# Performance work log

Measured on AMD Instinct MI355X. Metric: run time of the kernel, lower is better.

The kernel has to match this reference:

```python
import jax, jax.numpy as jnp
import numpy as np

L, B, D = 2048, 2, 1024
H, DK, DV = 16, 64, 64
SPAN = 128
LN_EPS = 1e-5


def setup_inputs() -> dict:
    key = jax.random.key(0)
    ks = jax.random.split(key, 8)
    s_qk = np.sqrt(2.0 / (D + DK)).astype(np.float32)
    s_v = np.sqrt(2.0 / (D + DV)).astype(np.float32)
    return {
        "query": jax.random.normal(ks[0], (L, B, D), jnp.float32),
        "key": jax.random.normal(ks[1], (L, B, D), jnp.float32),
        "value": jax.random.normal(ks[2], (L, B, D), jnp.float32),
        "Wq": jax.random.normal(ks[3], (D, H * DK), jnp.float32) * s_qk,
        "bq": jnp.zeros((H * DK,), jnp.float32),
        "Wk": jax.random.normal(ks[4], (D, H * DK), jnp.float32) * s_qk,
        "bk": jnp.zeros((H * DK,), jnp.float32),
        "Wv": jax.random.normal(ks[5], (D, H * DV), jnp.float32) * s_v,
        "bv": jnp.zeros((H * DV,), jnp.float32),
        "Wfc": jax.random.normal(ks[6], (H * DV, D), jnp.float32) * np.sqrt(2.0 / (H * DV + D)).astype(np.float32),
        "bfc": jnp.zeros((D,), jnp.float32),
        "gamma": jnp.ones((D,), jnp.float32),
        "beta": jnp.zeros((D,), jnp.float32),
    }


def reference(query, key, value, Wq, bq, Wk, bk, Wv, bv, Wfc, bfc, gamma, beta):
    l, b, d = query.shape
    # projections: (l,b,H*dk) -> (H,b,l,dk)   [torch rearrange 'l b (head k) -> head b l k']
    q = (query @ Wq + bq).reshape(l, b, H, DK).transpose(2, 1, 0, 3)
    k = (key @ Wk + bk).reshape(l, b, H, DK).transpose(2, 1, 0, 3)
    v = (value @ Wv + bv).reshape(l, b, H, DV).transpose(2, 1, 0, 3)
    scores = jnp.einsum("hblk,hbtk->hblt", q, k) / jnp.sqrt(jnp.float32(DK))
    # banded additive mask: keep |j - i| <= SPAN
    idx = jnp.arange(l)
    band = jnp.abs(idx[None, :] - idx[:, None]) <= SPAN  # (l, l)
    scores = jnp.where(band[None, None], scores, -jnp.inf)
    attn = jax.nn.softmax(scores, axis=-1)
    out = jnp.einsum("hblt,hbtv->hblv", attn, v)
    # 'head b l v -> l b (head v)'
    out = out.transpose(2, 1, 0, 3).reshape(l, b, H * DV)
    out = out @ Wfc + bfc  # dropout p=0.0 -> identity
    y = out + query  # residual
    mu = jnp.mean(y, axis=-1, keepdims=True)
    var = jnp.mean(jnp.square(y - mu), axis=-1, keepdims=True)
    y = (y - mu) * jax.lax.rsqrt(var + LN_EPS) * gamma + beta
    return (y, attn)
```

## Files before the change

kernel.cpp:

```cpp
#include <hip/hip_runtime.h>
#include <stdint.h>

#define L_SEQ 2048
#define BB 2
#define DD 1024
#define NH 16
#define SPAN 128

typedef __attribute__((ext_vector_type(8))) short short8;
typedef __attribute__((ext_vector_type(4))) float floatx4;

__device__ __forceinline__ short f32_bf16(float f) {
  uint32_t u = __float_as_uint(f);
  u += 0x7FFFu + ((u >> 16) & 1u);
  return (short)(u >> 16);
}
__device__ __forceinline__ float bf2f(short s) {
  return __uint_as_float(((uint32_t)(uint16_t)s) << 16);
}

__device__ __forceinline__ void gld16(const short* g, short* l) {
  __builtin_amdgcn_global_load_lds(
      (__attribute__((address_space(1))) void*)(g),
      (__attribute__((address_space(3))) void*)(l), 16, 0, 0);
}

__global__ __launch_bounds__(256) void k_prep(
    const float* __restrict__ s0, const float* __restrict__ s1, const float* __restrict__ s2,
    const float* __restrict__ w0, const float* __restrict__ w1,
    const float* __restrict__ w2, const float* __restrict__ w3,
    short* __restrict__ d0, short* __restrict__ d1, short* __restrict__ d2,
    short* __restrict__ WT) {
  __shared__ float tile[32][33];
  int bid = blockIdx.x, tid = threadIdx.x;
  if (bid < 12288) {
    int y = bid >> 12;
    const float* s = y == 0 ? s0 : (y == 1 ? s1 : s2);
    short* d = y == 0 ? d0 : (y == 1 ? d1 : d2);
    int i = (bid & 4095) * 256 + tid;
    float4 v = ((const float4*)s)[i];
    short4 o;
    o.x = f32_bf16(v.x); o.y = f32_bf16(v.y); o.z = f32_bf16(v.z); o.w = f32_bf16(v.w);
    ((short4*)d)[i] = o;
  } else {
    int b2 = bid - 12288;
    int z = b2 >> 10;
    int xy = b2 & 1023;
    int bx = (xy & 31) * 32, by = (xy >> 5) * 32;
    int tx = tid & 31, ty = tid >> 5;
    const float* src = z == 0 ? w0 : z == 1 ? w1 : z == 2 ? w2 : w3;
    short* out = WT + (size_t)z * (DD * DD);
#pragma unroll
    for (int r = 0; r < 32; r += 8)
      tile[ty + r][tx] = src[(size_t)(by + ty + r) * DD + bx + tx];
    __syncthreads();
#pragma unroll
    for (int r = 0; r < 32; r += 8)
      out[(size_t)(bx + ty + r) * DD + by + tx] = f32_bf16(tile[tx][ty + r]);
  }
}

#define BM 128
#define BN 128

__device__ __forceinline__ void gemm_core(const short* __restrict__ A,
                                          const short* __restrict__ BT,
                                          floatx4 acc[4][4], int bm0, int bn0) {
  __shared__ short As0[BM * 32], As1[BM * 32];
  __shared__ short Bs0[BN * 32], Bs1[BN * 32];
  int tid = threadIdx.x;
  int wave = tid >> 6, lane = tid & 63;
  int li = lane & 15, quad = lane >> 4;
  int wm = (wave & 1) * 64, wn = (wave >> 1) * 64;
  int r0 = wave * 32 + (lane >> 2);
  int c0 = (lane & 3) * 8;
  const short* gA = A + (size_t)(bm0 + r0) * DD + c0;
  const short* gB = BT + (size_t)(bn0 + r0) * DD + c0;
  short* lA0 = &As0[wave * 32 * 32];
  short* lA1 = &As1[wave * 32 * 32];
  short* lB0 = &Bs0[wave * 32 * 32];
  short* lB1 = &Bs1[wave * 32 * 32];
  for (int k0 = 0; k0 < DD; k0 += 64) {
    __syncthreads();
    gld16(gA + k0, lA0);
    gld16(gA + (size_t)16 * DD + k0, lA0 + 16 * 32);
    gld16(gA + k0 + 32, lA1);
    gld16(gA + (size_t)16 * DD + k0 + 32, lA1 + 16 * 32);
    gld16(gB + k0, lB0);
    gld16(gB + (size_t)16 * DD + k0, lB0 + 16 * 32);
    gld16(gB + k0 + 32, lB1);
    gld16(gB + (size_t)16 * DD + k0 + 32, lB1 + 16 * 32);
    __syncthreads();
    short8 af[4], bf[4];
#pragma unroll
    for (int t = 0; t < 4; ++t) {
      af[t] = *(const short8*)&As0[(wm + t * 16 + li) * 32 + quad * 8];
      bf[t] = *(const short8*)&Bs0[(wn + t * 16 + li) * 32 + quad * 8];
    }
#pragma unroll
    for (int tm = 0; tm < 4; ++tm)
#pragma unroll
      for (int tn = 0; tn < 4; ++tn)
        acc[tm][tn] = __builtin_amdgcn_mfma_f32_16x16x32_bf16(af[tm], bf[tn], acc[tm][tn], 0, 0, 0);
#pragma unroll
    for (int t = 0; t < 4; ++t) {
      af[t] = *(const short8*)&As1[(wm + t * 16 + li) * 32 + quad * 8];
      bf[t] = *(const short8*)&Bs1[(wn + t * 16 + li) * 32 + quad * 8];
    }
#pragma unroll
    for (int tm = 0; tm < 4; ++tm)
#pragma unroll
      for (int tn = 0; tn < 4; ++tn)
        acc[tm][tn] = __builtin_amdgcn_mfma_f32_16x16x32_bf16(af[tm], bf[tn], acc[tm][tn], 0, 0, 0);
  }
}

__global__ __launch_bounds__(256) void k_proj(
    const short* __restrict__ xq, const short* __restrict__ xk, const short* __restrict__ xv,
    const short* __restrict__ WT,
    const float* __restrict__ bq, const float* __restrict__ bk, const float* __restrict__ bv,
    short* __restrict__ qo, short* __restrict__ ko, short* __restrict__ vo) {
  int mode = blockIdx.z;
  const short* A = mode == 0 ? xq : (mode == 1 ? xk : xv);
  const short* BT = WT + (size_t)mode * DD * DD;
  const float* bias = mode == 0 ? bq : (mode == 1 ? bk : bv);
  floatx4 acc[4][4] = {};
  int bm0 = blockIdx.y * BM, bn0 = blockIdx.x * BN;
  gemm_core(A, BT, acc, bm0, bn0);

  int tid = threadIdx.x;
  int wave = tid >> 6, lane = tid & 63;
  int li = lane & 15, quad = lane >> 4;
  int wm = (wave & 1) * 64, wn = (wave >> 1) * 64;
  short* dst = (mode == 0) ? qo : (mode == 1 ? ko : vo);
#pragma unroll
  for (int tm = 0; tm < 4; ++tm) {
#pragma unroll
    for (int tn = 0; tn < 4; ++tn) {
      int gn = bn0 + wn + tn * 16 + li;
      float bs = bias[gn];
      int h = gn >> 6, dk = gn & 63;
#pragma unroll
      for (int r = 0; r < 4; ++r) {
        int gm = bm0 + wm + tm * 16 + quad * 4 + r;
        int l = gm >> 1, b = gm & 1;
        dst[(((size_t)h * BB + b) * L_SEQ + l) * 64 + dk] = f32_bf16(acc[tm][tn][r] + bs);
      }
    }
  }
}

__global__ __launch_bounds__(256) void k_vt(const short* __restrict__ vl, short* __restrict__ vt) {
  __shared__ short tl[64][72];
  int l0 = blockIdx.x * 64, hb = blockIdx.y;
  const short* src = vl + ((size_t)hb * L_SEQ + l0) * 64;
  short* dst = vt + (size_t)hb * 64 * L_SEQ + l0;
  int tid = threadIdx.x;
  int r = tid >> 2, c0 = (tid & 3) * 16;
  *(short8*)&tl[r][c0] = *(const short8*)(src + (size_t)r * 64 + c0);
  *(short8*)&tl[r][c0 + 8] = *(const short8*)(src + (size_t)r * 64 + c0 + 8);
  __syncthreads();
  int d = tid >> 2, lb = (tid & 3) * 16;
  short8 o0, o1;
#pragma unroll
  for (int j = 0; j < 8; ++j) o0[j] = tl[lb + j][d];
#pragma unroll
  for (int j = 0; j < 8; ++j) o1[j] = tl[lb + 8 + j][d];
  *(short8*)(dst + (size_t)d * L_SEQ + lb) = o0;
  *(short8*)(dst + (size_t)d * L_SEQ + lb + 8) = o1;
}

__global__ __launch_bounds__(256) void k_attn(
    const short* __restrict__ qw, const short* __restrict__ kw, const short* __restrict__ vTw,
    float* __restrict__ attn_out, short* __restrict__ ctx) {
  __shared__ short sbuf[20480];
  short* K0 = sbuf;
  short* K1 = sbuf + 10240;
  const int tid = threadIdx.x;
  const int wv = tid >> 6, lane = tid & 63;
  const int li = lane & 15, quad = lane >> 4;
  const int i0b = blockIdx.x * 64;
  const int i0 = i0b + wv * 16;
  const int jb = i0b - SPAN;
  const int hb = blockIdx.y;
  const short* Q = qw + (size_t)hb * L_SEQ * 64;
  const short* K = kw + (size_t)hb * L_SEQ * 64;
  const short* VT = vTw + (size_t)hb * 64 * L_SEQ;
  float* Aout = attn_out + (size_t)hb * L_SEQ * L_SEQ;

#pragma unroll
  for (int t = 0; t < 10; ++t) {
    int idx = wv + 4 * t;
    int half = idx >= 20 ? 1 : 0;
    int ridx = idx - half * 20;
    int row = ridx * 16 + (lane >> 2);
    int jr = jb + row;
    int jc = jr < 0 ? 0 : (jr >= L_SEQ ? L_SEQ - 1 : jr);
    const short* g = K + (size_t)jc * 64 + half * 32 + (lane & 3) * 8;
    short* l = (half ? K1 : K0) + ridx * 16 * 32;
    gld16(g, l);
  }

  short8 qf0 = *(const short8*)(Q + (size_t)(i0 + li) * 64 + quad * 8);
  short8 qf1 = *(const short8*)(Q + (size_t)(i0 + li) * 64 + 32 + quad * 8);
  __syncthreads();

  floatx4 S[17];
  const int jbase = i0 - SPAN;
#pragma unroll
  for (int t = 0; t < 17; ++t) {
    int j0 = jbase + t * 16;
    floatx4 acc = {0.f, 0.f, 0.f, 0.f};
    if (j0 > -16 && j0 < L_SEQ) {
      int jrel = (wv + t) * 16;
      short8 kf0 = *(const short8*)&K0[(jrel + li) * 32 + quad * 8];
      short8 kf1 = *(const short8*)&K1[(jrel + li) * 32 + quad * 8];
      acc = __builtin_amdgcn_mfma_f32_16x16x32_bf16(qf0, kf0, acc, 0, 0, 0);
      acc = __builtin_amdgcn_mfma_f32_16x16x32_bf16(qf1, kf1, acc, 0, 0, 0);
    }
    S[t] = acc;
  }
  float mrow[4] = {-1e30f, -1e30f, -1e30f, -1e30f};
#pragma unroll
  for (int t = 0; t < 17; ++t) {
    int j = jbase + t * 16 + li;
#pragma unroll
    for (int r = 0; r < 4; ++r) {
      int i = i0 + quad * 4 + r;
      bool inband = (j >= i - SPAN) && (j <= i + SPAN) && (j >= 0) && (j < L_SEQ);
      float s = inband ? S[t][r] * 0.125f : -1e30f;
      S[t][r] = s;
      mrow[r] = fmaxf(mrow[r], s);
    }
  }
#pragma unroll
  for (int m = 1; m <= 8; m <<= 1)
#pragma unroll
    for (int r = 0; r < 4; ++r) mrow[r] = fmaxf(mrow[r], __shfl_xor(mrow[r], m));
  float lsum[4] = {0.f, 0.f, 0.f, 0.f};
#pragma unroll
  for (int t = 0; t < 17; ++t)
#pragma unroll
    for (int r = 0; r < 4; ++r) {
      float p = __expf(S[t][r] - mrow[r]);
      S[t][r] = p;
      lsum[r] += p;
    }
#pragma unroll
  for (int m = 1; m <= 8; m <<= 1)
#pragma unroll
    for (int r = 0; r < 4; ++r) lsum[r] += __shfl_xor(lsum[r], m);
  float inv[4];
#pragma unroll
  for (int r = 0; r < 4; ++r) inv[r] = 1.0f / lsum[r];

  __syncthreads();
  short* myP = sbuf + wv * 4736;
#pragma unroll
  for (int t = 0; t < 17; ++t)
#pragma unroll
    for (int r = 0; r < 4; ++r)
      myP[(quad * 4 + r) * 296 + t * 16 + li] = f32_bf16(S[t][r] * inv[r]);
  *(short4*)&myP[(lane >> 2) * 296 + 272 + (lane & 3) * 4] = short4{0, 0, 0, 0};
  __syncthreads();

  floatx4 O[4] = {};
#pragma unroll
  for (int c = 0; c < 9; ++c) {
    short8 pf = *(const short8*)&myP[li * 296 + c * 32 + quad * 8];
    int jg = jbase + c * 32 + quad * 8;
    int jc = (jg >= 0 && jg < L_SEQ) ? jg : 0;
#pragma unroll
    for (int n = 0; n < 4; ++n) {
      short8 vf = *(const short8*)(VT + (size_t)(n * 16 + li) * L_SEQ + jc);
      O[n] = __builtin_amdgcn_mfma_f32_16x16x32_bf16(pf, vf, O[n], 0, 0, 0);
    }
  }
  const int b = hb & 1, h = hb >> 1;
#pragma unroll
  for (int n = 0; n < 4; ++n)
#pragma unroll
    for (int r = 0; r < 4; ++r) {
      int irow = quad * 4 + r;
      ctx[((size_t)(i0 + irow) * BB + b) * DD + h * 64 + n * 16 + li] = f32_bf16(O[n][r]);
    }

#pragma unroll 4
  for (int row = 0; row < 16; ++row) {
    float* orow = Aout + (size_t)(i0 + row) * L_SEQ;
    const short* prow = &myP[row * 296];
#pragma unroll
    for (int it = 0; it < 8; ++it) {
      int col = it * 256 + lane * 4;
      int s = col - jbase;
      floatx4 v = {0.f, 0.f, 0.f, 0.f};
      if (s >= 0 && s < 288) {
        short4 p4 = *(const short4*)(prow + s);
        v.x = bf2f(p4.x); v.y = bf2f(p4.y); v.z = bf2f(p4.z); v.w = bf2f(p4.w);
      }
      __builtin_nontemporal_store(v, (floatx4*)(orow + col));
    }
  }
}

__global__ __launch_bounds__(256) void k_fc(
    const short* __restrict__ ctx, const short* __restrict__ WfcT,
    const float* __restrict__ bfc, const float* __restrict__ query,
    float* __restrict__ ypre) {
  floatx4 acc[4][4] = {};
  int bm0 = blockIdx.y * BM, bn0 = blockIdx.x * BN;
  gemm_core(ctx, WfcT, acc, bm0, bn0);
  int tid = threadIdx.x;
  int wave = tid >> 6, lane = tid & 63;
  int li = lane & 15, quad = lane >> 4;
  int wm = (wave & 1) * 64, wn = (wave >> 1) * 64;
#pragma unroll
  for (int tm = 0; tm < 4; ++tm)
#pragma unroll
    for (int tn = 0; tn < 4; ++tn) {
      int gn = bn0 + wn + tn * 16 + li;
      float bs = bfc[gn];
#pragma unroll
      for (int r = 0; r < 4; ++r) {
        int gm = bm0 + wm + tm * 16 + quad * 4 + r;
        ypre[(size_t)gm * DD + gn] = acc[tm][tn][r] + bs + query[(size_t)gm * DD + gn];
      }
    }
}

__global__ __launch_bounds__(256) void k_ln(
    const float* __restrict__ yp, const float* __restrict__ gamma,
    const float* __restrict__ beta, float* __restrict__ out) {
  __shared__ float red[8];
  int row = blockIdx.x, tid = threadIdx.x;
  float4 v = ((const float4*)(yp + (size_t)row * DD))[tid];
  float s = v.x + v.y + v.z + v.w;
  float s2 = v.x * v.x + v.y * v.y + v.z * v.z + v.w * v.w;
#pragma unroll
  for (int m = 1; m <= 32; m <<= 1) {
    s += __shfl_xor(s, m);
    s2 += __shfl_xor(s2, m);
  }
  int wv = tid >> 6;
  if ((tid & 63) == 0) { red[wv] = s; red[wv + 4] = s2; }
  __syncthreads();
  s = red[0] + red[1] + red[2] + red[3];
  s2 = red[4] + red[5] + red[6] + red[7];
  float mu = s * (1.0f / DD);
  float var = s2 * (1.0f / DD) - mu * mu;
  float rs = rsqrtf(var + 1e-5f);
  float4 g = ((const float4*)gamma)[tid];
  float4 bb = ((const float4*)beta)[tid];
  float4 o;
  o.x = (v.x - mu) * rs * g.x + bb.x;
  o.y = (v.y - mu) * rs * g.y + bb.y;
  o.z = (v.z - mu) * rs * g.z + bb.z;
  o.w = (v.w - mu) * rs * g.w + bb.w;
  ((float4*)(out + (size_t)row * DD))[tid] = o;
}

extern "C" void kernel_launch(void* const* d_in, const int* in_sizes, int n_in,
                              void* d_out, int out_size, void* d_ws, size_t ws_size,
                              hipStream_t stream) {
  const float* query = (const float*)d_in[0];
  const float* key   = (const float*)d_in[1];
  const float* value = (const float*)d_in[2];
  const float* Wq    = (const float*)d_in[3];
  const float* bq    = (const float*)d_in[4];
  const float* Wk    = (const float*)d_in[5];
  const float* bk    = (const float*)d_in[6];
  const float* Wv    = (const float*)d_in[7];
  const float* bv    = (const float*)d_in[8];
  const float* Wfc   = (const float*)d_in[9];
  const float* bfc   = (const float*)d_in[10];
  const float* gamma = (const float*)d_in[11];
  const float* beta  = (const float*)d_in[12];
  float* out = (float*)d_out;
  float* attn = out + (size_t)L_SEQ * BB * DD;

  char* w = (char*)d_ws;
  short* xq_b  = (short*)(w);
  short* xk_b  = (short*)(w + ((size_t)8 << 20));
  short* xv_b  = (short*)(w + ((size_t)16 << 20));
  short* WT    = (short*)(w + ((size_t)24 << 20));
  short* q_ws  = (short*)(w + ((size_t)32 << 20));
  short* k_ws  = (short*)(w + ((size_t)40 << 20));
  short* v_lin = (short*)(w + ((size_t)48 << 20));
  short* vT_ws = (short*)(w + ((size_t)56 << 20));
  short* ctx   = (short*)(w + ((size_t)64 << 20));
  float* ypre  = (float*)(w + ((size_t)72 << 20));

  k_prep<<<16384, 256, 0, stream>>>(query, key, value, Wq, Wk, Wv, Wfc,
                                    xq_b, xk_b, xv_b, WT);
  k_proj<<<dim3(8, 32, 3), 256, 0, stream>>>(xq_b, xk_b, xv_b, WT, bq, bk, bv, q_ws, k_ws, v_lin);
  k_vt<<<dim3(32, 32), 256, 0, stream>>>(v_lin, vT_ws);
  k_attn<<<dim3(32, 32), 256, 0, stream>>>(q_ws, k_ws, vT_ws, attn, ctx);
  k_fc<<<dim3(8, 32), 256, 0, stream>>>(ctx, WT + (size_t)3 * DD * DD, bfc, query, ypre);
  k_ln<<<4096, 256, 0, stream>>>(ypre, gamma, beta, out);
}
```

Measured before the change: 712.0 us.

## Vectorize transposes and epilogues, double-buffer GEMM, swizzle blocks, add MFMA priority

Weight transpose in the prep kernel now uses 64x64 tiles with 16-byte bf16 stores. The GEMM core moves to a ping-pong LDS prefetch with one barrier per K-step of 32. Projection and FC epilogues stage results through LDS so global writes and residual reads are coalesced vectors. Block indices in projection, attention and FC are swizzled for cache locality, and attention raises wave priority around MFMA sections with V fragments loaded ahead. This trades extra LDS traffic and barriers for fewer scattered global accesses.

```diff
diff --git a/kernel.cpp b/kernel.cpp
--- a/kernel.cpp
+++ b/kernel.cpp
@@ -31,7 +31,7 @@
     const float* __restrict__ w2, const float* __restrict__ w3,
     short* __restrict__ d0, short* __restrict__ d1, short* __restrict__ d2,
     short* __restrict__ WT) {
-  __shared__ float tile[32][33];
+  __shared__ float tile[64][65];
   int bid = blockIdx.x, tid = threadIdx.x;
   if (bid < 12288) {
     int y = bid >> 12;
@@ -44,30 +44,35 @@
     ((short4*)d)[i] = o;
   } else {
     int b2 = bid - 12288;
-    int z = b2 >> 10;
-    int xy = b2 & 1023;
-    int bx = (xy & 31) * 32, by = (xy >> 5) * 32;
-    int tx = tid & 31, ty = tid >> 5;
+    int z = b2 >> 8;
+    int xy = b2 & 255;
+    int bx = (xy & 15) * 64, by = (xy >> 4) * 64;
+    int tx = tid & 63, ty = tid >> 6;
     const float* src = z == 0 ? w0 : z == 1 ? w1 : z == 2 ? w2 : w3;
     short* out = WT + (size_t)z * (DD * DD);
 #pragma unroll
-    for (int r = 0; r < 32; r += 8)
+    for (int r = 0; r < 64; r += 4)
       tile[ty + r][tx] = src[(size_t)(by + ty + r) * DD + bx + tx];
     __syncthreads();
-#pragma unroll
-    for (int r = 0; r < 32; r += 8)
-      out[(size_t)(bx + ty + r) * DD + by + tx] = f32_bf16(tile[tx][ty + r]);
+    int r2 = tid >> 2, q = tid & 3;
+    short8 o0, o1;
+#pragma unroll
+    for (int j = 0; j < 8; ++j) o0[j] = f32_bf16(tile[q * 16 + j][r2]);
+#pragma unroll
+    for (int j = 0; j < 8; ++j) o1[j] = f32_bf16(tile[q * 16 + 8 + j][r2]);
+    *(short8*)(out + (size_t)(bx + r2) * DD + by + q * 16) = o0;
+    *(short8*)(out + (size_t)(bx + r2) * DD + by + q * 16 + 8) = o1;
   }
 }
 
 #define BM 128
 #define BN 128
+#define SMEM_SH 17408
 
 __device__ __forceinline__ void gemm_core(const short* __restrict__ A,
                                           const short* __restrict__ BT,
-                                          floatx4 acc[4][4], int bm0, int bn0) {
-  __shared__ short As0[BM * 32], As1[BM * 32];
-  __shared__ short Bs0[BN * 32], Bs1[BN * 32];
+                                          floatx4 acc[4][4], int bm0, int bn0,
+                                          short* smem) {
   int tid = threadIdx.x;
   int wave = tid >> 6, lane = tid & 63;
   int li = lane & 15, quad = lane >> 4;
@@ -76,42 +81,43 @@
   int c0 = (lane & 3) * 8;
   const short* gA = A + (size_t)(bm0 + r0) * DD + c0;
   const short* gB = BT + (size_t)(bn0 + r0) * DD + c0;
-  short* lA0 = &As0[wave * 32 * 32];
-  short* lA1 = &As1[wave * 32 * 32];
-  short* lB0 = &Bs0[wave * 32 * 32];
-  short* lB1 = &Bs1[wave * 32 * 32];
-  for (int k0 = 0; k0 < DD; k0 += 64) {
-    __syncthreads();
-    gld16(gA + k0, lA0);
-    gld16(gA + (size_t)16 * DD + k0, lA0 + 16 * 32);
-    gld16(gA + k0 + 32, lA1);
-    gld16(gA + (size_t)16 * DD + k0 + 32, lA1 + 16 * 32);
-    gld16(gB + k0, lB0);
-    gld16(gB + (size_t)16 * DD + k0, lB0 + 16 * 32);
-    gld16(gB + k0 + 32, lB1);
-    gld16(gB + (size_t)16 * DD + k0 + 32, lB1 + 16 * 32);
-    __syncthreads();
+  short* sA = smem;
+  short* sB = smem + 8192;
+  {
+    short* lA = sA + wave * 1024;
+    short* lB = sB + wave * 1024;
+    gld16(gA, lA);
+    gld16(gA + (size_t)16 * DD, lA + 512);
+    gld16(gB, lB);
+    gld16(gB + (size_t)16 * DD, lB + 512);
+  }
+  __syncthreads();
+#pragma unroll 2
+  for (int k = 0; k < 32; ++k) {
+    int cur = k & 1;
+    if (k < 31) {
+      int koff = (k + 1) * 32;
+      short* lA = sA + (cur ^ 1) * 4096 + wave * 1024;
+      short* lB = sB + (cur ^ 1) * 4096 + wave * 1024;
+      gld16(gA + koff, lA);
+      gld16(gA + (size_t)16 * DD + koff, lA + 512);
+      gld16(gB + koff, lB);
+      gld16(gB + (size_t)16 * DD + koff, lB + 512);
+    }
+    const short* cA = sA + cur * 4096;
+    const short* cB = sB + cur * 4096;
     short8 af[4], bf[4];
 #pragma unroll
     for (int t = 0; t < 4; ++t) {
-      af[t] = *(const short8*)&As0[(wm + t * 16 + li) * 32 + quad * 8];
-      bf[t] = *(const short8*)&Bs0[(wn + t * 16 + li) * 32 + quad * 8];
+      af[t] = *(const short8*)&cA[(wm + t * 16 + li) * 32 + quad * 8];
+      bf[t] = *(const short8*)&cB[(wn + t * 16 + li) * 32 + quad * 8];
     }
 #pragma unroll
     for (int tm = 0; tm < 4; ++tm)
 #pragma unroll
       for (int tn = 0; tn < 4; ++tn)
         acc[tm][tn] = __builtin_amdgcn_mfma_f32_16x16x32_bf16(af[tm], bf[tn], acc[tm][tn], 0, 0, 0);
-#pragma unroll
-    for (int t = 0; t < 4; ++t) {
-      af[t] = *(const short8*)&As1[(wm + t * 16 + li) * 32 + quad * 8];
-      bf[t] = *(const short8*)&Bs1[(wn + t * 16 + li) * 32 + quad * 8];
-    }
-#pragma unroll
-    for (int tm = 0; tm < 4; ++tm)
-#pragma unroll
-      for (int tn = 0; tn < 4; ++tn)
-        acc[tm][tn] = __builtin_amdgcn_mfma_f32_16x16x32_bf16(af[tm], bf[tn], acc[tm][tn], 0, 0, 0);
+    __syncthreads();
   }
 }
 
@@ -120,13 +126,16 @@
     const short* __restrict__ WT,
     const float* __restrict__ bq, const float* __restrict__ bk, const float* __restrict__ bv,
     short* __restrict__ qo, short* __restrict__ ko, short* __restrict__ vo) {
-  int mode = blockIdx.z;
+  __shared__ __attribute__((aligned(16))) short smem[SMEM_SH];
+  int flat = (blockIdx.z * 32 + blockIdx.y) * 8 + blockIdx.x;
+  int swz = (flat & 7) * 96 + (flat >> 3);
+  int bxw = swz & 7, byw = (swz >> 3) & 31, mode = swz >> 8;
   const short* A = mode == 0 ? xq : (mode == 1 ? xk : xv);
   const short* BT = WT + (size_t)mode * DD * DD;
   const float* bias = mode == 0 ? bq : (mode == 1 ? bk : bv);
   floatx4 acc[4][4] = {};
-  int bm0 = blockIdx.y * BM, bn0 = blockIdx.x * BN;
-  gemm_core(A, BT, acc, bm0, bn0);
+  int bm0 = byw * BM, bn0 = bxw * BN;
+  gemm_core(A, BT, acc, bm0, bn0, smem);
 
   int tid = threadIdx.x;
   int wave = tid >> 6, lane = tid & 63;
@@ -134,20 +143,24 @@
   int wm = (wave & 1) * 64, wn = (wave >> 1) * 64;
   short* dst = (mode == 0) ? qo : (mode == 1 ? ko : vo);
 #pragma unroll
-  for (int tm = 0; tm < 4; ++tm) {
+  for (int tm = 0; tm < 4; ++tm)
 #pragma unroll
     for (int tn = 0; tn < 4; ++tn) {
       int gn = bn0 + wn + tn * 16 + li;
       float bs = bias[gn];
-      int h = gn >> 6, dk = gn & 63;
-#pragma unroll
-      for (int r = 0; r < 4; ++r) {
-        int gm = bm0 + wm + tm * 16 + quad * 4 + r;
-        int l = gm >> 1, b = gm & 1;
-        dst[(((size_t)h * BB + b) * L_SEQ + l) * 64 + dk] = f32_bf16(acc[tm][tn][r] + bs);
-      }
-    }
-  }
+#pragma unroll
+      for (int r = 0; r < 4; ++r)
+        smem[(wm + tm * 16 + quad * 4 + r) * 136 + wn + tn * 16 + li] =
+            f32_bf16(acc[tm][tn][r] + bs);
+    }
+  __syncthreads();
+  int row = tid >> 1, half = tid & 1;
+  int gm = bm0 + row, l = gm >> 1, b = gm & 1;
+  int h = (bn0 + half * 64) >> 6;
+  short* drow = dst + (((size_t)h * BB + b) * L_SEQ + l) * 64;
+#pragma unroll
+  for (int j = 0; j < 8; ++j)
+    *(short8*)(drow + j * 8) = *(const short8*)&smem[row * 136 + half * 64 + j * 8];
 }
 
 __global__ __launch_bounds__(256) void k_vt(const short* __restrict__ vl, short* __restrict__ vt) {
@@ -179,10 +192,12 @@
   const int tid = threadIdx.x;
   const int wv = tid >> 6, lane = tid & 63;
   const int li = lane & 15, quad = lane >> 4;
-  const int i0b = blockIdx.x * 64;
+  int flat = blockIdx.y * 32 + blockIdx.x;
+  int swz = (flat & 7) * 128 + (flat >> 3);
+  const int i0b = (swz & 31) * 64;
+  const int hb = swz >> 5;
   const int i0 = i0b + wv * 16;
   const int jb = i0b - SPAN;
-  const int hb = blockIdx.y;
   const short* Q = qw + (size_t)hb * L_SEQ * 64;
   const short* K = kw + (size_t)hb * L_SEQ * 64;
   const short* VT = vTw + (size_t)hb * 64 * L_SEQ;
@@ -207,6 +222,7 @@
 
   floatx4 S[17];
   const int jbase = i0 - SPAN;
+  __builtin_amdgcn_s_setprio(1);
 #pragma unroll
   for (int t = 0; t < 17; ++t) {
     int j0 = jbase + t * 16;
@@ -220,6 +236,7 @@
     }
     S[t] = acc;
   }
+  __builtin_amdgcn_s_setprio(0);
   float mrow[4] = {-1e30f, -1e30f, -1e30f, -1e30f};
 #pragma unroll
   for (int t = 0; t < 17; ++t) {
@@ -270,11 +287,15 @@
     short8 pf = *(const short8*)&myP[li * 296 + c * 32 + quad * 8];
     int jg = jbase + c * 32 + quad * 8;
     int jc = (jg >= 0 && jg < L_SEQ) ? jg : 0;
-#pragma unroll
-    for (int n = 0; n < 4; ++n) {
-      short8 vf = *(const short8*)(VT + (size_t)(n * 16 + li) * L_SEQ + jc);
-      O[n] = __builtin_amdgcn_mfma_f32_16x16x32_bf16(pf, vf, O[n], 0, 0, 0);
-    }
+    short8 vf[4];
+#pragma unroll
+    for (int n = 0; n < 4; ++n)
+      vf[n] = *(const short8*)(VT + (size_t)(n * 16 + li) * L_SEQ + jc);
+    __builtin_amdgcn_s_setprio(1);
+#pragma unroll
+    for (int n = 0; n < 4; ++n)
+      O[n] = __builtin_amdgcn_mfma_f32_16x16x32_bf16(pf, vf[n], O[n], 0, 0, 0);
+    __builtin_amdgcn_s_setprio(0);
   }
   const int b = hb & 1, h = hb >> 1;
 #pragma unroll
@@ -307,25 +328,46 @@
     const short* __restrict__ ctx, const short* __restrict__ WfcT,
     const float* __restrict__ bfc, const float* __restrict__ query,
     float* __restrict__ ypre) {
+  __shared__ __attribute__((aligned(16))) short smem[SMEM_SH];
+  int flat = blockIdx.y * 8 + blockIdx.x;
+  int swz = (flat & 7) * 32 + (flat >> 3);
+  int bm0 = (swz >> 3) * BM, bn0 = (swz & 7) * BN;
   floatx4 acc[4][4] = {};
-  int bm0 = blockIdx.y * BM, bn0 = blockIdx.x * BN;
-  gemm_core(ctx, WfcT, acc, bm0, bn0);
+  gemm_core(ctx, WfcT, acc, bm0, bn0, smem);
   int tid = threadIdx.x;
   int wave = tid >> 6, lane = tid & 63;
   int li = lane & 15, quad = lane >> 4;
-  int wm = (wave & 1) * 64, wn = (wave >> 1) * 64;
-#pragma unroll
-  for (int tm = 0; tm < 4; ++tm)
-#pragma unroll
-    for (int tn = 0; tn < 4; ++tn) {
-      int gn = bn0 + wn + tn * 16 + li;
-      float bs = bfc[gn];
-#pragma unroll
-      for (int r = 0; r < 4; ++r) {
-        int gm = bm0 + wm + tm * 16 + quad * 4 + r;
-        ypre[(size_t)gm * DD + gn] = acc[tm][tn][r] + bs + query[(size_t)gm * DD + gn];
-      }
-    }
+  int wn = (wave >> 1) * 64;
+  float* ft = (float*)smem;
+#pragma unroll
+  for (int hrow = 0; hrow < 2; ++hrow) {
+    __syncthreads();
+    if ((wave & 1) == hrow) {
+#pragma unroll
+      for (int tm = 0; tm < 4; ++tm)
+#pragma unroll
+        for (int tn = 0; tn < 4; ++tn) {
+          int gn = bn0 + wn + tn * 16 + li;
+          float bs = bfc[gn];
+#pragma unroll
+          for (int r = 0; r < 4; ++r)
+            ft[(tm * 16 + quad * 4 + r) * 136 + wn + tn * 16 + li] = acc[tm][tn][r] + bs;
+        }
+    }
+    __syncthreads();
+    int row = tid >> 2, c0 = (tid & 3) * 32;
+    int gm = bm0 + hrow * 64 + row;
+    const float4* q4 = (const float4*)(query + (size_t)gm * DD + bn0 + c0);
+    float4* o4 = (float4*)(ypre + (size_t)gm * DD + bn0 + c0);
+#pragma unroll
+    for (int v = 0; v < 8; ++v) {
+      float4 a = *(const float4*)&ft[row * 136 + c0 + v * 4];
+      float4 qq = q4[v];
+      float4 o;
+      o.x = a.x + qq.x; o.y = a.y + qq.y; o.z = a.z + qq.z; o.w = a.w + qq.w;
+      o4[v] = o;
+    }
+  }
 }
 
 __global__ __launch_bounds__(256) void k_ln(
@@ -390,7 +432,7 @@
   short* ctx   = (short*)(w + ((size_t)64 << 20));
   float* ypre  = (float*)(w + ((size_t)72 << 20));
 
-  k_prep<<<16384, 256, 0, stream>>>(query, key, value, Wq, Wk, Wv, Wfc,
+  k_prep<<<13312, 256, 0, stream>>>(query, key, value, Wq, Wk, Wv, Wfc,
                                     xq_b, xk_b, xv_b, WT);
   k_proj<<<dim3(8, 32, 3), 256, 0, stream>>>(xq_b, xk_b, xv_b, WT, bq, bk, bv, q_ws, k_ws, v_lin);
   k_vt<<<dim3(32, 32), 256, 0, stream>>>(v_lin, vT_ws);
```

After: 705.5 us. No clear change (-0.9%).
